# Kernel optimization log

Hardware: AMD Instinct MI355X
Metric: run time of the kernel (lower is better)

## Reference

```python
import jax, jax.numpy as jnp
import numpy as np

COMMITMENT_COST = 0.25


def setup_inputs() -> dict:
    key = jax.random.key(0)
    k1, k2 = jax.random.split(key)
    B, S, D, K = 64, 512, 512, 4096
    inputs = jax.random.normal(k1, (B, S, D), dtype=jnp.float32)
    # codebook initialized uniform(-1/K, 1/K) like the torch module
    codebook = jax.random.uniform(k2, (K, D), dtype=jnp.float32,
                                  minval=-1.0 / K, maxval=1.0 / K)
    return {"inputs": inputs, "codebook": codebook}


def reference(inputs, codebook):
    D = inputs.shape[-1]
    flat = inputs.reshape(-1, D)  # [N, D]
    # squared euclidean distances to every code: [N, K]
    dist = (jnp.sum(flat * flat, axis=1, keepdims=True)
            + jnp.sum(codebook * codebook, axis=1)
            - 2.0 * flat @ codebook.T)
    idx = jnp.argmin(dist, axis=1)  # [N]
    # gather replaces one-hot scatter + matmul (same math)
    quantized = codebook[idx].reshape(inputs.shape)
    commitment_loss = jnp.mean((jax.lax.stop_gradient(quantized) - inputs) ** 2)
    codebook_loss = jnp.mean((quantized - jax.lax.stop_gradient(inputs)) ** 2)
    quantize_loss = COMMITMENT_COST * commitment_loss + codebook_loss
    # straight-through estimator
    quantized_st = inputs + jax.lax.stop_gradient(quantized - inputs)
    encoding_indices = idx.reshape(inputs.shape[:-1])
    return quantized_st, quantize_loss, encoding_indices
```

## Files before the change

### kernel.cpp

```cpp
#include <hip/hip_runtime.h>

#define N_ROWS 32768
#define DIM    512
#define KCODES 4096
#define NPARTS 16
#define KPART  (KCODES / NPARTS)
#define Q_ELEMS (N_ROWS * DIM)
#define LOSS_OFF Q_ELEMS
#define IDX_OFF (Q_ELEMS + 1)

__global__ void k_init(unsigned long long* __restrict__ bk) {
    int i = blockIdx.x * blockDim.x + threadIdx.x;
    if (i < N_ROWS) bk[i] = 0xFFFFFFFFFFFFFFFFull;
}

__global__ void k_cnorm(const float* __restrict__ cb, float* __restrict__ cnorm) {
    int wave = (blockIdx.x * blockDim.x + threadIdx.x) >> 6;
    int lane = threadIdx.x & 63;
    if (wave >= KCODES) return;
    const float4* row = (const float4*)(cb + (size_t)wave * DIM);
    float4 v1 = row[lane];
    float4 v2 = row[lane + 64];
    float s = v1.x*v1.x + v1.y*v1.y + v1.z*v1.z + v1.w*v1.w
            + v2.x*v2.x + v2.y*v2.y + v2.z*v2.z + v2.w*v2.w;
    #pragma unroll
    for (int m = 32; m >= 1; m >>= 1) s += __shfl_xor(s, m);
    if (lane == 0) cnorm[wave] = s;
}

__global__ void k_xnorm(const float* __restrict__ x, float* __restrict__ xnorm) {
    int wave = (blockIdx.x * blockDim.x + threadIdx.x) >> 6;
    int lane = threadIdx.x & 63;
    if (wave >= N_ROWS) return;
    const float4* row = (const float4*)(x + (size_t)wave * DIM);
    float4 v1 = row[lane];
    float4 v2 = row[lane + 64];
    float s = v1.x*v1.x + v1.y*v1.y + v1.z*v1.z + v1.w*v1.w
            + v2.x*v2.x + v2.y*v2.y + v2.z*v2.z + v2.w*v2.w;
    #pragma unroll
    for (int m = 32; m >= 1; m >>= 1) s += __shfl_xor(s, m);
    if (lane == 0) xnorm[wave] = s;
}

#define BM 128
#define BN 128
#define BD 32
#define NTHR 256
#define NCH ((KPART / BN) * (DIM / BD))

__global__ __launch_bounds__(NTHR)
void k_argmin(const float* __restrict__ x, const float* __restrict__ cb,
              const float* __restrict__ cnorm, const float* __restrict__ xnorm,
              unsigned long long* __restrict__ bestkey) {
    __shared__ float xs[BM][BD + 4];
    __shared__ float cs[BD][BN];

    const int tid = threadIdx.x;
    const int ty = tid >> 4;
    const int tx = tid & 15;
    const int r0 = blockIdx.x * BM;
    const int kbase = blockIdx.y * KPART;

    const int ck   = tid & 127;
    const int cdq0 = tid >> 7;

    float xn[8];
    #pragma unroll
    for (int i = 0; i < 8; ++i) xn[i] = xnorm[r0 + ty + 16 * i];

    float best[8];
    int   bidx[8];
    #pragma unroll
    for (int i = 0; i < 8; ++i) { best[i] = 3.4e38f; bidx[i] = kbase; }

    float acc[8][8];

    #pragma unroll 1
    for (int it = 0; it < NCH; ++it) {
        const int kc = it >> 4;
        const int dc = (it & 15) * BD;

        __syncthreads();
        #pragma unroll
        for (int s = 0; s < 4; ++s) {
            int f = tid + s * NTHR;
            int row = f >> 3;
            int dq  = f & 7;
            *(float4*)&xs[row][dq * 4] =
                *(const float4*)(x + (size_t)(r0 + row) * DIM + dc + dq * 4);
        }
        #pragma unroll
        for (int it2 = 0; it2 < 4; ++it2) {
            int dq = cdq0 + it2 * 2;
            float4 v = *(const float4*)(cb + (size_t)(kbase + kc * BN + ck) * DIM + dc + dq * 4);
            cs[dq * 4 + 0][ck] = v.x;
            cs[dq * 4 + 1][ck] = v.y;
            cs[dq * 4 + 2][ck] = v.z;
            cs[dq * 4 + 3][ck] = v.w;
        }
        __syncthreads();

        if ((it & 15) == 0) {
            #pragma unroll
            for (int i = 0; i < 8; ++i)
                #pragma unroll
                for (int j = 0; j < 8; ++j) acc[i][j] = 0.f;
        }

        #pragma unroll
        for (int d4 = 0; d4 < 8; ++d4) {
            float4 xa[8];
            #pragma unroll
            for (int i = 0; i < 8; ++i)
                xa[i] = *(const float4*)&xs[ty + 16 * i][d4 * 4];
            #pragma unroll
            for (int dd = 0; dd < 4; ++dd) {
                int d = d4 * 4 + dd;
                float4 b0 = *(const float4*)&cs[d][tx * 4];
                float4 b1 = *(const float4*)&cs[d][64 + tx * 4];
                #pragma unroll
                for (int i = 0; i < 8; ++i) {
                    float a = (dd == 0) ? xa[i].x : (dd == 1) ? xa[i].y
                            : (dd == 2) ? xa[i].z : xa[i].w;
                    acc[i][0] = fmaf(a, b0.x, acc[i][0]);
                    acc[i][1] = fmaf(a, b0.y, acc[i][1]);
                    acc[i][2] = fmaf(a, b0.z, acc[i][2]);
                    acc[i][3] = fmaf(a, b0.w, acc[i][3]);
                    acc[i][4] = fmaf(a, b1.x, acc[i][4]);
                    acc[i][5] = fmaf(a, b1.y, acc[i][5]);
                    acc[i][6] = fmaf(a, b1.z, acc[i][6]);
                    acc[i][7] = fmaf(a, b1.w, acc[i][7]);
                }
            }
        }

        if ((it & 15) == 15) {
            #pragma unroll
            for (int half = 0; half < 2; ++half) {
                #pragma unroll
                for (int j = 0; j < 4; ++j) {
                    int k = kbase + kc * BN + half * 64 + tx * 4 + j;
                    float cn = cnorm[k];
                    #pragma unroll
                    for (int i = 0; i < 8; ++i) {
                        float t1 = xn[i] + cn;
                        float tw = 2.0f * acc[i][half * 4 + j];
                        float s  = t1 - tw;
                        if (s < best[i]) { best[i] = s; bidx[i] = k; }
                    }
                }
            }
        }
    }

    #pragma unroll
    for (int i = 0; i < 8; ++i) {
        float b = best[i];
        int   ix = bidx[i];
        #pragma unroll
        for (int m = 1; m <= 8; m <<= 1) {
            float ob = __shfl_xor(b, m);
            int   oi = __shfl_xor(ix, m);
            if (ob < b || (ob == b && oi < ix)) { b = ob; ix = oi; }
        }
        if (tx == 0) {
            int row = r0 + ty + 16 * i;
            unsigned int ub = __float_as_uint(b);
            ub = (ub & 0x80000000u) ? ~ub : (ub | 0x80000000u);
            unsigned long long key = ((unsigned long long)ub << 32) | (unsigned int)ix;
            atomicMin(bestkey + row, key);
        }
    }
}

__global__ void k_gather(const float* __restrict__ x, const float* __restrict__ cb,
                         const unsigned long long* __restrict__ bestkey,
                         float* __restrict__ qout, float* __restrict__ idx_out,
                         float* __restrict__ partial) {
    int row  = blockIdx.x * 4 + (threadIdx.x >> 6);
    int lane = threadIdx.x & 63;
    int bk = (int)(bestkey[row] & 0xFFFFFFFFull);
    if (lane == 0) idx_out[row] = (float)bk;
    const float4* crow = (const float4*)(cb + (size_t)bk * DIM);
    const float4* xrow = (const float4*)(x + (size_t)row * DIM);
    float4* qrow = (float4*)(qout + (size_t)row * DIM);
    float s = 0.f;
    #pragma unroll
    for (int it = 0; it < 2; ++it) {
        int d4 = lane + it * 64;
        float4 q = crow[d4];
        float4 xi = xrow[d4];
        qrow[d4] = q;
        float dx = q.x - xi.x; s += dx * dx;
        dx = q.y - xi.y; s += dx * dx;
        dx = q.z - xi.z; s += dx * dx;
        dx = q.w - xi.w; s += dx * dx;
    }
    #pragma unroll
    for (int m = 32; m >= 1; m >>= 1) s += __shfl_xor(s, m);
    __shared__ float ws4[4];
    if (lane == 0) ws4[threadIdx.x >> 6] = s;
    __syncthreads();
    if (threadIdx.x == 0)
        partial[blockIdx.x] = (ws4[0] + ws4[1]) + (ws4[2] + ws4[3]);
}

__global__ void k_loss(const float* __restrict__ partial, float* __restrict__ out_loss) {
    int t = threadIdx.x;
    double s = 0.0;
    #pragma unroll 4
    for (int i = 0; i < 32; ++i) s += (double)partial[t * 32 + i];
    #pragma unroll
    for (int m = 32; m >= 1; m >>= 1) s += __shfl_xor(s, m);
    __shared__ double sd[4];
    if ((t & 63) == 0) sd[t >> 6] = s;
    __syncthreads();
    if (t == 0) {
        double tot = (sd[0] + sd[1]) + (sd[2] + sd[3]);
        out_loss[0] = (float)(1.25 * tot / (double)Q_ELEMS);
    }
}

extern "C" void kernel_launch(void* const* d_in, const int* in_sizes, int n_in,
                              void* d_out, int out_size, void* d_ws, size_t ws_size,
                              hipStream_t stream) {
    const float* x  = (const float*)d_in[0];
    const float* cb = (const float*)d_in[1];
    float* out = (float*)d_out;

    char* ws = (char*)d_ws;
    unsigned long long* bestkey = (unsigned long long*)ws;  ws += (size_t)N_ROWS * 8;
    float* cnorm = (float*)ws;                              ws += (size_t)KCODES * 4;
    float* xnorm = (float*)ws;                              ws += (size_t)N_ROWS * 4;
    float* part  = (float*)ws;

    k_init<<<N_ROWS / 256, 256, 0, stream>>>(bestkey);
    k_cnorm<<<KCODES / 4, 256, 0, stream>>>(cb, cnorm);
    k_xnorm<<<N_ROWS / 4, 256, 0, stream>>>(x, xnorm);
    dim3 agrid(N_ROWS / BM, NPARTS);
    k_argmin<<<agrid, NTHR, 0, stream>>>(x, cb, cnorm, xnorm, bestkey);
    k_gather<<<N_ROWS / 4, 256, 0, stream>>>(x, cb, bestkey, out, out + IDX_OFF, part);
    k_loss<<<1, 256, 0, stream>>>(part, out + LOSS_OFF);
}
```

Measured before the change: 1.659 ms.

## Double-buffer codebook tiles via register prefetch and read x directly from global

```diff
diff --git a/kernel.cpp b/kernel.cpp
--- a/kernel.cpp
+++ b/kernel.cpp
@@ -52,8 +52,7 @@
 void k_argmin(const float* __restrict__ x, const float* __restrict__ cb,
               const float* __restrict__ cnorm, const float* __restrict__ xnorm,
               unsigned long long* __restrict__ bestkey) {
-    __shared__ float xs[BM][BD + 4];
-    __shared__ float cs[BD][BN];
+    __shared__ float cs[2][BD][BN];
 
     const int tid = threadIdx.x;
     const int ty = tid >> 4;
@@ -74,31 +73,38 @@
     for (int i = 0; i < 8; ++i) { best[i] = 3.4e38f; bidx[i] = kbase; }
 
     float acc[8][8];
+    float4 cr[4];
+
+    #pragma unroll
+    for (int it2 = 0; it2 < 4; ++it2) {
+        int dq = cdq0 + it2 * 2;
+        cr[it2] = *(const float4*)(cb + (size_t)(kbase + ck) * DIM + dq * 4);
+    }
+    #pragma unroll
+    for (int it2 = 0; it2 < 4; ++it2) {
+        int dq = cdq0 + it2 * 2;
+        cs[0][dq * 4 + 0][ck] = cr[it2].x;
+        cs[0][dq * 4 + 1][ck] = cr[it2].y;
+        cs[0][dq * 4 + 2][ck] = cr[it2].z;
+        cs[0][dq * 4 + 3][ck] = cr[it2].w;
+    }
+    __syncthreads();
 
     #pragma unroll 1
     for (int it = 0; it < NCH; ++it) {
+        const int b  = it & 1;
         const int kc = it >> 4;
         const int dc = (it & 15) * BD;
 
-        __syncthreads();
-        #pragma unroll
-        for (int s = 0; s < 4; ++s) {
-            int f = tid + s * NTHR;
-            int row = f >> 3;
-            int dq  = f & 7;
-            *(float4*)&xs[row][dq * 4] =
-                *(const float4*)(x + (size_t)(r0 + row) * DIM + dc + dq * 4);
-        }
-        #pragma unroll
-        for (int it2 = 0; it2 < 4; ++it2) {
-            int dq = cdq0 + it2 * 2;
-            float4 v = *(const float4*)(cb + (size_t)(kbase + kc * BN + ck) * DIM + dc + dq * 4);
-            cs[dq * 4 + 0][ck] = v.x;
-            cs[dq * 4 + 1][ck] = v.y;
-            cs[dq * 4 + 2][ck] = v.z;
-            cs[dq * 4 + 3][ck] = v.w;
-        }
-        __syncthreads();
+        if (it + 1 < NCH) {
+            const int nkc = (it + 1) >> 4;
+            const int ndc = ((it + 1) & 15) * BD;
+            #pragma unroll
+            for (int it2 = 0; it2 < 4; ++it2) {
+                int dq = cdq0 + it2 * 2;
+                cr[it2] = *(const float4*)(cb + (size_t)(kbase + nkc * BN + ck) * DIM + ndc + dq * 4);
+            }
+        }
 
         if ((it & 15) == 0) {
             #pragma unroll
@@ -112,12 +118,12 @@
             float4 xa[8];
             #pragma unroll
             for (int i = 0; i < 8; ++i)
-                xa[i] = *(const float4*)&xs[ty + 16 * i][d4 * 4];
+                xa[i] = *(const float4*)(x + (size_t)(r0 + ty + 16 * i) * DIM + dc + d4 * 4);
             #pragma unroll
             for (int dd = 0; dd < 4; ++dd) {
                 int d = d4 * 4 + dd;
-                float4 b0 = *(const float4*)&cs[d][tx * 4];
-                float4 b1 = *(const float4*)&cs[d][64 + tx * 4];
+                float4 b0 = *(const float4*)&cs[b][d][tx * 4];
+                float4 b1 = *(const float4*)&cs[b][d][64 + tx * 4];
                 #pragma unroll
                 for (int i = 0; i < 8; ++i) {
                     float a = (dd == 0) ? xa[i].x : (dd == 1) ? xa[i].y
@@ -151,6 +157,18 @@
                 }
             }
         }
+
+        if (it + 1 < NCH) {
+            #pragma unroll
+            for (int it2 = 0; it2 < 4; ++it2) {
+                int dq = cdq0 + it2 * 2;
+                cs[b ^ 1][dq * 4 + 0][ck] = cr[it2].x;
+                cs[b ^ 1][dq * 4 + 1][ck] = cr[it2].y;
+                cs[b ^ 1][dq * 4 + 2][ck] = cr[it2].z;
+                cs[b ^ 1][dq * 4 + 3][ck] = cr[it2].w;
+            }
+            __syncthreads();
+        }
     }
 
     #pragma unroll
```

New measurement: 2.072 ms. 1.25x slower.
